# Kernel tuning notes

Hardware: AMD Instinct MI355X
Metric: run time of the kernel (lower is better)

The kernel has to match this reference:

```python
import jax, jax.numpy as jnp
from jax import lax
import numpy as np

# Constants from CVLNet utils (get_meter_per_pixel() and SatMap_original_sidelength)
METER_PER_PIXEL = 0.2
SATMAP_ORIGINAL_SIDELENGTH = 512.0
SHIFT_RANGE = 32
EPS = 1e-12


def _l2_normalize_per_sample(x):
    # F.normalize(x.reshape(B, -1)) : L2-normalize each sample over all elements
    B = x.shape[0]
    norm = jnp.linalg.norm(x.reshape(B, -1), axis=1)
    norm = jnp.maximum(norm, EPS).reshape((B,) + (1,) * (x.ndim - 1))
    return x / norm


def setup_inputs() -> dict:
    key = jax.random.key(0)
    k1, k2 = jax.random.split(key)
    grd_feature = jax.random.normal(k1, (4, 32, 64, 64), dtype=jnp.float32)   # (N,C,Hk,Wk)
    sat_feature = jax.random.normal(k2, (32, 32, 64, 64), dtype=jnp.float32)  # (M,C,Hs,Ws)
    return {"grd_feature": grd_feature, "sat_feature": sat_feature, "uncertainty": 1}


def reference(grd_feature, sat_feature, uncertainty):
    N, C, H_k, W_k = grd_feature.shape
    grd = _l2_normalize_per_sample(grd_feature)

    s = SHIFT_RANGE
    sat = jnp.pad(sat_feature, ((0, 0), (0, 0), (s, s), (s, s)))
    M, _, H_i, W_i = sat.shape
    sat = _l2_normalize_per_sample(sat)  # zero-padding does not change the norm

    # F.conv2d(sat.repeat(1,N,1,1), grd, groups=N) == plain cross-correlation of
    # every sat map with every grd template: output [M, N, Ho, Wo]
    corr = lax.conv_general_dilated(
        sat, grd, window_strides=(1, 1), padding='VALID',
        dimension_numbers=('NCHW', 'OIHW', 'NCHW'))

    # avg_pool2d(sat^2, (Hk,Wk), stride=1, divisor_override=1) summed over C ==
    # sliding-window sum of per-pixel squared norms
    s2 = jnp.sum(sat * sat, axis=1, keepdims=True)  # [M,1,Hi,Wi]
    partical = lax.reduce_window(s2, 0.0, lax.add,
                                 window_dimensions=(1, 1, H_k, W_k),
                                 window_strides=(1, 1, 1, 1), padding='VALID')
    denom = jnp.maximum(jnp.sqrt(partical) * uncertainty, EPS)
    corr = corr / denom

    similarity_matrix = jnp.max(corr, axis=(2, 3))  # [M,N]

    Wo = corr.shape[-1]
    max_index = jnp.argmax(corr.reshape(M, N, -1), axis=-1)
    row = (max_index // Wo).astype(jnp.float32)
    col = (max_index % Wo).astype(jnp.float32)
    half = Wo / 2.0
    max_pos = jnp.stack([-(row - half), col - half], axis=-1)  # [M,N,2]
    shift_meters = max_pos * METER_PER_PIXEL * SATMAP_ORIGINAL_SIDELENGTH / W_i
    return (similarity_matrix, shift_meters)
```

## Files before the change

### kernel.cpp

```cpp
#include <hip/hip_runtime.h>
#include <math.h>

#define N_GRD 4
#define M_SAT 32
#define C_CH  32
#define HK    64
#define WK    64
#define HO    65
#define WO    65
#define SAMPLE_ELEMS (C_CH * HK * WK)

typedef _Float16 h8 __attribute__((ext_vector_type(8)));
typedef float    f4 __attribute__((ext_vector_type(4)));
typedef unsigned int u32;

#define OFF_INV    0
#define OFF_S      64
#define OFF_CANDV  135264
#define OFF_CANDI  135776
#define OFF_DOTS   136288
#define OFF_PART   136800
#define OFF_G2F    956000
#define OFF_SH     1824352
#define G2_HALFS   1736704

#define G2_BLOCKS  6784
#define SH_BLOCKS  2048
#define PREP_BLOCKS (G2_BLOCKS + SH_BLOCKS + M_SAT + N_GRD)

__global__ __launch_bounds__(256) void prep_kernel(const float* __restrict__ grd,
                                                   const float* __restrict__ sat,
                                                   _Float16* __restrict__ g2,
                                                   _Float16* __restrict__ sh,
                                                   float* __restrict__ S,
                                                   float* __restrict__ inv) {
    const int bx = blockIdx.x;
    const int tid = threadIdx.x;
    __shared__ float s2[64][65];

    if (bx < G2_BLOCKS) {
        int idx = bx * 256 + tid;
        int c = idx & 3; int t = idx >> 2;
        int js = t % 106; t /= 106;
        int n = t & 3; t >>= 2;
        int i = t & 63; t >>= 6;
        int cq = t & 7; int cp = t >> 3;
        int j = js - 16 - cp;
        float v = 0.0f;
        if (j >= 0 && j < 64)
            v = grd[(((size_t)n * 32 + (cq * 4 + c)) * 64 + i) * 64 + j];
        g2[idx] = (_Float16)v;
        return;
    }
    if (bx < G2_BLOCKS + SH_BLOCKS) {
        int idx = (bx - G2_BLOCKS) * 256 + tid;
        int gr = idx & 31;
        int r  = (idx >> 5) & 63;
        int cq = (idx >> 11) & 7;
        int mm = idx >> 14;
        const float* sp = sat + (((size_t)mm * 32 + cq * 4) * 64 + r) * 64 + gr * 2;
        float2 v0 = *(const float2*)(sp);
        float2 v1 = *(const float2*)(sp + 4096);
        float2 v2 = *(const float2*)(sp + 8192);
        float2 v3 = *(const float2*)(sp + 12288);
        h8 hv = {(_Float16)v0.x, (_Float16)v1.x, (_Float16)v2.x, (_Float16)v3.x,
                 (_Float16)v0.y, (_Float16)v1.y, (_Float16)v2.y, (_Float16)v3.y};
        *(h8*)(sh + (size_t)idx * 8) = hv;
        return;
    }
    if (bx < G2_BLOCKS + SH_BLOCKS + M_SAT) {
        const int m = bx - G2_BLOCKS - SH_BLOCKS;
        const float* base = sat + (size_t)m * SAMPLE_ELEMS;
        for (int p = tid; p < HK * WK; p += 256) {
            float s = 0.0f;
            for (int c = 0; c < C_CH; ++c) {
                float v = base[c * (HK * WK) + p];
                s += v * v;
            }
            s2[p >> 6][p & 63] = s;
        }
        __syncthreads();
        if (tid < 64) {
            int r = tid; float run = 0.0f;
            for (int w = 0; w < 64; ++w) { run += s2[r][w]; s2[r][w] = run; }
        }
        __syncthreads();
        if (tid < 64) {
            int c = tid; float run = 0.0f;
            for (int h = 0; h < 64; ++h) { run += s2[h][c]; s2[h][c] = run; }
        }
        __syncthreads();
        if (tid == 0)
            inv[N_GRD + m] = 1.0f / fmaxf(sqrtf(s2[63][63]), 1e-12f);
        float* Sm = S + (size_t)m * (HO * WO);
        for (int p = tid; p < HO * WO; p += 256) {
            int r = p / 65, c = p - r * 65;
            Sm[p] = (r == 0 || c == 0) ? 0.0f : s2[r - 1][c - 1];
        }
        return;
    }
    {
        const int b = bx - G2_BLOCKS - SH_BLOCKS - M_SAT;
        const float4* v = reinterpret_cast<const float4*>(grd + (size_t)b * SAMPLE_ELEMS);
        float ss = 0.0f;
        for (int p = tid; p < SAMPLE_ELEMS / 4; p += 256) {
            float4 q = v[p];
            ss += q.x * q.x + q.y * q.y + q.z * q.z + q.w * q.w;
        }
        for (int off = 32; off > 0; off >>= 1) ss += __shfl_down(ss, off);
        __shared__ float ls[4];
        int lane = tid & 63, w = tid >> 6;
        if (lane == 0) ls[w] = ss;
        __syncthreads();
        if (tid == 0)
            inv[b] = 1.0f / fmaxf(sqrtf(ls[0] + ls[1] + ls[2] + ls[3]), 1e-12f);
    }
}

__global__ __launch_bounds__(256, 2) void corr_mfma_kernel(const _Float16* __restrict__ sh,
                                                           const _Float16* __restrict__ g2,
                                                           float* __restrict__ partial) {
    __shared__ __align__(16) char lds[75520];
    char* AB = lds;
    char* BB = lds + 48384;

    const int m  = blockIdx.x;
    const int xs = blockIdx.y;
    const int z  = blockIdx.z;
    const int h  = z & 1;
    const int qt = z >> 1;

    const int x00 = (xs < 4) ? 16 * xs : 49;
    const int qb  = (xs < 4) ? 16 * xs : 48;
    const int xoff = x00 - qb;
    const int qstage = qb + 40 * h;

    const int tid  = threadIdx.x;
    const int w    = tid >> 6;
    const int lane = tid & 63;
    const int s    = lane & 15;
    const int u    = lane >> 4;
    const int cp   = (s + xoff) & 1;

    f4 acc[5][4];
#pragma unroll
    for (int t = 0; t < 5; ++t)
#pragma unroll
        for (int n = 0; n < 4; ++n) { acc[t][n][0]=0.f; acc[t][n][1]=0.f; acc[t][n][2]=0.f; acc[t][n][3]=0.f; }

    const int bbase = ((w * 2 + cp) * 4 * 106 + (16 + cp + 40 * h + 2 * u - s - xoff)) * 8;
    const int abase0 = s * 336 + u * 16;
    const int q2base = qstage >> 1;

    for (int cqi = 0; cqi < 2; ++cqi) {
        const int cq = qt * 2 + cqi;
        __syncthreads();
        for (int k = 0; k < 11; ++k) {
            int idx = k * 256 + tid;
            if (idx < 2688) {
                u32 r = (u32)idx / 21u;
                u32 g = (u32)idx - r * 21u;
                int q2 = q2base + (int)g;
                bool valid = (g < 20u) & (r >= 32u) & (r < 96u) & (q2 >= 16) & (q2 < 48);
                const _Float16* src = valid
                    ? sh + ((((size_t)m * 8 + cq) * 64 + (r - 32)) * 32 + (q2 - 16)) * 8
                    : g2;
                __builtin_amdgcn_global_load_lds(
                    (const __attribute__((address_space(1))) u32*)(const void*)src,
                    (__attribute__((address_space(3))) u32*)(void*)(AB + k * 4096 + w * 1024),
                    16, 0, 0);
            }
        }
        for (int ii = 0; ii < 16; ++ii) {
            __syncthreads();
            for (int k = 0; k < 7; ++k) {
                int idx = k * 256 + tid;
                if (idx < 1696) {
                    int wi = idx / 424;  int rm  = idx - wi * 424;
                    int cpp = rm / 212;  int rm2 = rm - cpp * 212;
                    int nn = rm2 / 53;   int jg  = rm2 - nn * 53;
                    int iw = wi * 16 + ii;
                    const _Float16* gsrc = g2 + (size_t)((((cpp * 8 + cq) * 64 + iw) * 4 + nn)) * 424 + jg * 8;
                    __builtin_amdgcn_global_load_lds(
                        (const __attribute__((address_space(1))) u32*)(const void*)gsrc,
                        (__attribute__((address_space(3))) u32*)(void*)(BB + k * 4096 + w * 1024),
                        16, 0, 0);
                }
            }
            __syncthreads();
            const char* Ab = AB + abase0 + (w * 16 + ii) * 336;
            const char* Bb = BB + bbase;
#pragma unroll
            for (int qs = 0; qs < 5; ++qs) {
                h8 a[5]; h8 bfr[4];
#pragma unroll
                for (int n = 0; n < 4; ++n) bfr[n] = *(const h8*)(Bb + qs * 64 + n * 848);
#pragma unroll
                for (int t = 0; t < 5; ++t) a[t] = *(const h8*)(Ab + qs * 64 + t * 5376);
#pragma unroll
                for (int t = 0; t < 5; ++t)
#pragma unroll
                    for (int n = 0; n < 4; ++n)
                        acc[t][n] = __builtin_amdgcn_mfma_f32_16x16x32_f16(a[t], bfr[n], acc[t][n], 0, 0, 0);
            }
        }
    }

    float* red = (float*)lds;
#pragma unroll
    for (int t = 0; t < 5; ++t) {
        __syncthreads();
#pragma unroll
        for (int nn = 0; nn < 4; ++nn)
            *(f4*)(red + ((nn * 4 + w) * 64 + lane) * 4) = acc[t][nn];
        __syncthreads();
        {
            int nn = tid >> 6, ln = tid & 63;
            f4 sum = *(f4*)(red + ((nn * 4 + 0) * 64 + ln) * 4);
            sum = sum + *(f4*)(red + ((nn * 4 + 1) * 64 + ln) * 4);
            sum = sum + *(f4*)(red + ((nn * 4 + 2) * 64 + ln) * 4);
            sum = sum + *(f4*)(red + ((nn * 4 + 3) * 64 + ln) * 4);
            int ss = ln & 15, uu = ln >> 4;
            float* dst = partial + ((size_t)(m * 4 + nn)) * 6400
                         + (xs * 16 + ss) * 80 + t * 16 + uu * 4;
#pragma unroll
            for (int l = 0; l < 4; ++l) atomicAdd(dst + l, sum[l]);
        }
    }
}

__global__ __launch_bounds__(256) void epilogue_kernel(const float* __restrict__ partial,
                                                       const float* __restrict__ S,
                                                       const float* __restrict__ inv,
                                                       const int* __restrict__ unc,
                                                       float* __restrict__ candv,
                                                       int* __restrict__ candi) {
    const int b = blockIdx.x;
    const int m = b >> 2, n = b & 3;
    const int tid = threadIdx.x;
    const float uu = (float)unc[0];
    const float sc = inv[n] * inv[N_GRD + m];
    const float isn = inv[N_GRD + m];
    const float* Sm = S + (size_t)m * 4225;
    const float* pb = partial + (size_t)(m * 4 + n) * 6400;

    float best = -3.4e38f;
    int bidx = 0x7fffffff;
    for (int pp = tid; pp < 4225; pp += 256) {
        int x = pp / 65, y = pp - x * 65;
        int xsl = (x == 64) ? 79 : x;
        float raw = pb[xsl * 80 + y];
        float num = raw * sc;
        int r0 = max(0, y - 32), r1 = min(64, y + 32);
        int q0 = max(0, x - 32), q1 = min(64, x + 32);
        float ps = Sm[r1 * 65 + q1] - Sm[r0 * 65 + q1] - Sm[r1 * 65 + q0] + Sm[r0 * 65 + q0];
        float denom = fmaxf(sqrtf(ps) * isn * uu, 1e-12f);
        float v = num / denom;
        int p = y * 65 + x;
        if (v > best || (v == best && p < bidx)) { best = v; bidx = p; }
    }
    __shared__ float bv[256]; __shared__ int bi[256];
    __shared__ float cv[256]; __shared__ int ci[256];
    __shared__ int winner;
    bv[tid] = best; bi[tid] = bidx;
    __syncthreads();
    for (int round = 0; round < 4; ++round) {
        cv[tid] = bv[tid]; ci[tid] = bi[tid];
        __syncthreads();
        for (int st = 128; st > 0; st >>= 1) {
            if (tid < st) {
                float ov = cv[tid + st]; int oi = ci[tid + st];
                if (ov > cv[tid] || (ov == cv[tid] && oi < ci[tid])) { cv[tid] = ov; ci[tid] = oi; }
            }
            __syncthreads();
        }
        if (tid == 0) { candv[b * 4 + round] = cv[0]; candi[b * 4 + round] = ci[0]; winner = ci[0]; }
        __syncthreads();
        if (bi[tid] == winner) bv[tid] = -3.4e38f;
        __syncthreads();
    }
}

__global__ __launch_bounds__(256) void refine_dot_kernel(const float* __restrict__ grd,
                                                         const float* __restrict__ sat,
                                                         const float* __restrict__ candv,
                                                         const int* __restrict__ candi,
                                                         float* __restrict__ dots) {
    const int b = blockIdx.x;
    const int k = blockIdx.y;
    const int cq = blockIdx.z;
    const int m = b >> 2, n = b & 3;
    float v0 = candv[b * 4];
    float thr = v0 - (0.02f * fabsf(v0) + 1e-4f);
    if (k > 0 && candv[b * 4 + k] < thr) return;
    int p = candi[b * 4 + k];
    int y = p / 65, x = p - y * 65;
    const int tid = threadIdx.x, lane = tid & 63, w = tid >> 6;
    const int ilo = max(0, 32 - y), ihi = min(64, 96 - y);
    int xj = x + lane - 32;
    float acc = 0.0f;
    if (xj >= 0 && xj < 64) {
        const float* sm = sat + (size_t)m * SAMPLE_ELEMS;
        const float* gn = grd + (size_t)n * SAMPLE_ELEMS;
        for (int cc = 0; cc < 4; ++cc) {
            const int cbase = (cq * 4 + cc) << 12;
            const float* sp = sm + cbase + xj + ((y - 32) << 6);
            const float* gp = gn + cbase + lane;
            for (int i = ilo + w; i < ihi; i += 4)
                acc = fmaf(sp[i << 6], gp[i << 6], acc);
        }
    }
    for (int off = 32; off > 0; off >>= 1) acc += __shfl_down(acc, off);
    __shared__ float ls[4];
    if (lane == 0) ls[w] = acc;
    __syncthreads();
    if (tid == 0) atomicAdd(&dots[b * 4 + k], ls[0] + ls[1] + ls[2] + ls[3]);
}

__global__ __launch_bounds__(128) void refine_pick_kernel(const float* __restrict__ S,
                                                          const float* __restrict__ inv,
                                                          const int* __restrict__ unc,
                                                          const float* __restrict__ candv,
                                                          const int* __restrict__ candi,
                                                          const float* __restrict__ dots,
                                                          float* __restrict__ out) {
    int b = threadIdx.x;
    if (b >= 128) return;
    const int m = b >> 2, n = b & 3;
    const float uu = (float)unc[0];
    const float sc = inv[n] * inv[N_GRD + m];
    const float isn = inv[N_GRD + m];
    const float* Sm = S + (size_t)m * 4225;
    float v0 = candv[b * 4];
    float thr = v0 - (0.02f * fabsf(v0) + 1e-4f);
    float bestv = -3.4e38f; int bestp = 0x7fffffff;
    for (int k = 0; k < 4; ++k) {
        if (k > 0 && candv[b * 4 + k] < thr) break;
        int p = candi[b * 4 + k];
        int y = p / 65, x = p - y * 65;
        int r0 = max(0, y - 32), r1 = min(64, y + 32);
        int q0 = max(0, x - 32), q1 = min(64, x + 32);
        float ps = Sm[r1 * 65 + q1] - Sm[r0 * 65 + q1] - Sm[r1 * 65 + q0] + Sm[r0 * 65 + q0];
        float denom = fmaxf(sqrtf(ps) * isn * uu, 1e-12f);
        float v = dots[b * 4 + k] * sc / denom;
        if (v > bestv || (v == bestv && p < bestp)) { bestv = v; bestp = p; }
    }
    out[b] = bestv;
    int row = bestp / 65, col = bestp - row * 65;
    float pr = -((float)row - 32.5f);
    float pc = (float)col - 32.5f;
    out[128 + b * 2 + 0] = ((pr * 0.2f) * 512.0f) * (1.0f / 128.0f);
    out[128 + b * 2 + 1] = ((pc * 0.2f) * 512.0f) * (1.0f / 128.0f);
}

extern "C" void kernel_launch(void* const* d_in, const int* in_sizes, int n_in,
                              void* d_out, int out_size, void* d_ws, size_t ws_size,
                              hipStream_t stream) {
    const float* grd = (const float*)d_in[0];
    const float* sat = (const float*)d_in[1];
    const int*   unc = (const int*)d_in[2];
    float* out = (float*)d_out;
    float* ws  = (float*)d_ws;

    float* inv     = ws + OFF_INV;
    float* S       = ws + OFF_S;
    float* candv   = ws + OFF_CANDV;
    int*   candi   = (int*)(ws + OFF_CANDI);
    float* dots    = ws + OFF_DOTS;
    float* partial = ws + OFF_PART;
    _Float16* g2   = (_Float16*)(ws + OFF_G2F);
    _Float16* sh   = (_Float16*)(ws + OFF_SH);

    hipMemsetAsync(partial, 0, 819200 * sizeof(float), stream);
    hipMemsetAsync(dots, 0, 512 * sizeof(float), stream);
    prep_kernel<<<PREP_BLOCKS, 256, 0, stream>>>(grd, sat, g2, sh, S, inv);
    corr_mfma_kernel<<<dim3(M_SAT, 5, 8), 256, 0, stream>>>(sh, g2, partial);
    epilogue_kernel<<<M_SAT * N_GRD, 256, 0, stream>>>(partial, S, inv, unc, candv, candi);
    refine_dot_kernel<<<dim3(128, 4, 8), 256, 0, stream>>>(grd, sat, candv, candi, dots);
    refine_pick_kernel<<<1, 128, 0, stream>>>(S, inv, unc, candv, candi, dots, out);
}
```

Measured before the change: 377.5 us.

## Split ragged output edge into separate FP32 kernel, trim MFMA grid to 64x64

The MFMA correlation kernel previously covered a 65x65 output with a fifth x-slab (xs=4) and a fifth tile per block, and most of that extra work was wasted padding. It now computes only the 64x64 interior. A new FP32 edge kernel handles the last output row and column with direct dot products, exploiting the zero-padded sat region to limit the loop bounds. This removes a fifth of the MFMA blocks and shrinks per-block registers and LDS. The cost is an extra launch, slow scalar FP32 loads with atomics for the strips, and mixed precision between edge and interior.

```diff
diff --git a/kernel.cpp b/kernel.cpp
--- a/kernel.cpp
+++ b/kernel.cpp
@@ -117,12 +117,58 @@
     }
 }
 
+__global__ __launch_bounds__(256) void edge_kernel(const float* __restrict__ grd,
+                                                   const float* __restrict__ sat,
+                                                   float* __restrict__ partial) {
+    const int m = blockIdx.x, n = blockIdx.y;
+    const int strip = blockIdx.z & 1, ch = blockIdx.z >> 1;
+    const int tid = threadIdx.x, w = tid >> 6, lane = tid & 63;
+    const float* sm = sat + (size_t)m * SAMPLE_ELEMS + (size_t)ch * 16 * 4096;
+    const float* gn = grd + (size_t)n * SAMPLE_ELEMS + (size_t)ch * 16 * 4096;
+    float* pb = partial + (size_t)(m * 4 + n) * 6400;
+
+    if (strip == 0) {
+        const int j = lane & 31, sub = lane >> 5;
+        for (int pass = 0; pass < 9; ++pass) {
+            int yo = pass * 8 + w * 2 + sub;
+            float acc = 0.0f;
+            if (yo <= 64) {
+                int ilo = max(0, 32 - yo), ihi = min(64, 96 - yo);
+                for (int i = ilo; i < ihi; ++i) {
+#pragma unroll
+                    for (int c = 0; c < 16; ++c)
+                        acc = fmaf(sm[c * 4096 + (yo - 32 + i) * 64 + 32 + j],
+                                   gn[c * 4096 + i * 64 + j], acc);
+                }
+            }
+            for (int off = 16; off > 0; off >>= 1) acc += __shfl_down(acc, off, 32);
+            if (j == 0 && yo <= 64) atomicAdd(pb + 79 * 80 + yo, acc);
+        }
+    } else {
+        for (int pass = 0; pass < 16; ++pass) {
+            int xo = pass * 4 + w;
+            int xj = xo + lane - 32;
+            float acc = 0.0f;
+            if (xj >= 0 && xj < 64) {
+                for (int i = 0; i < 32; ++i) {
+#pragma unroll
+                    for (int c = 0; c < 16; ++c)
+                        acc = fmaf(sm[c * 4096 + (32 + i) * 64 + xj],
+                                   gn[c * 4096 + i * 64 + lane], acc);
+                }
+            }
+            for (int off = 32; off > 0; off >>= 1) acc += __shfl_down(acc, off);
+            if (lane == 0) atomicAdd(pb + xo * 80 + 64, acc);
+        }
+    }
+}
+
 __global__ __launch_bounds__(256, 2) void corr_mfma_kernel(const _Float16* __restrict__ sh,
                                                            const _Float16* __restrict__ g2,
                                                            float* __restrict__ partial) {
-    __shared__ __align__(16) char lds[75520];
+    __shared__ __align__(16) char lds[70144];
     char* AB = lds;
-    char* BB = lds + 48384;
+    char* BB = lds + 43008;
 
     const int m  = blockIdx.x;
     const int xs = blockIdx.y;
@@ -130,9 +176,7 @@
     const int h  = z & 1;
     const int qt = z >> 1;
 
-    const int x00 = (xs < 4) ? 16 * xs : 49;
-    const int qb  = (xs < 4) ? 16 * xs : 48;
-    const int xoff = x00 - qb;
+    const int qb  = 16 * xs;
     const int qstage = qb + 40 * h;
 
     const int tid  = threadIdx.x;
@@ -140,15 +184,15 @@
     const int lane = tid & 63;
     const int s    = lane & 15;
     const int u    = lane >> 4;
-    const int cp   = (s + xoff) & 1;
-
-    f4 acc[5][4];
-#pragma unroll
-    for (int t = 0; t < 5; ++t)
+    const int cp   = s & 1;
+
+    f4 acc[4][4];
+#pragma unroll
+    for (int t = 0; t < 4; ++t)
 #pragma unroll
         for (int n = 0; n < 4; ++n) { acc[t][n][0]=0.f; acc[t][n][1]=0.f; acc[t][n][2]=0.f; acc[t][n][3]=0.f; }
 
-    const int bbase = ((w * 2 + cp) * 4 * 106 + (16 + cp + 40 * h + 2 * u - s - xoff)) * 8;
+    const int bbase = ((w * 2 + cp) * 4 * 106 + (16 + cp + 40 * h + 2 * u - s)) * 8;
     const int abase0 = s * 336 + u * 16;
     const int q2base = qstage >> 1;
 
@@ -192,13 +236,13 @@
             const char* Bb = BB + bbase;
 #pragma unroll
             for (int qs = 0; qs < 5; ++qs) {
-                h8 a[5]; h8 bfr[4];
+                h8 a[4]; h8 bfr[4];
 #pragma unroll
                 for (int n = 0; n < 4; ++n) bfr[n] = *(const h8*)(Bb + qs * 64 + n * 848);
 #pragma unroll
-                for (int t = 0; t < 5; ++t) a[t] = *(const h8*)(Ab + qs * 64 + t * 5376);
-#pragma unroll
-                for (int t = 0; t < 5; ++t)
+                for (int t = 0; t < 4; ++t) a[t] = *(const h8*)(Ab + qs * 64 + t * 5376);
+#pragma unroll
+                for (int t = 0; t < 4; ++t)
 #pragma unroll
                     for (int n = 0; n < 4; ++n)
                         acc[t][n] = __builtin_amdgcn_mfma_f32_16x16x32_f16(a[t], bfr[n], acc[t][n], 0, 0, 0);
@@ -208,7 +252,7 @@
 
     float* red = (float*)lds;
 #pragma unroll
-    for (int t = 0; t < 5; ++t) {
+    for (int t = 0; t < 4; ++t) {
         __syncthreads();
 #pragma unroll
         for (int nn = 0; nn < 4; ++nn)
@@ -373,8 +417,9 @@
 
     hipMemsetAsync(partial, 0, 819200 * sizeof(float), stream);
     hipMemsetAsync(dots, 0, 512 * sizeof(float), stream);
+    edge_kernel<<<dim3(M_SAT, N_GRD, 4), 256, 0, stream>>>(grd, sat, partial);
     prep_kernel<<<PREP_BLOCKS, 256, 0, stream>>>(grd, sat, g2, sh, S, inv);
-    corr_mfma_kernel<<<dim3(M_SAT, 5, 8), 256, 0, stream>>>(sh, g2, partial);
+    corr_mfma_kernel<<<dim3(M_SAT, 4, 8), 256, 0, stream>>>(sh, g2, partial);
     epilogue_kernel<<<M_SAT * N_GRD, 256, 0, stream>>>(partial, S, inv, unc, candv, candi);
     refine_dot_kernel<<<dim3(128, 4, 8), 256, 0, stream>>>(grd, sat, candv, candi, dots);
     refine_pick_kernel<<<1, 128, 0, stream>>>(S, inv, unc, candv, candi, dots, out);
```

Result: slower. 605.2 us (+60.3%).
